# Kernel tuning notes

Hardware: AMD Instinct MI355X
Metric: run time of the kernel (lower is better)

Reference implementation:

```python
import jax, jax.numpy as jnp
import numpy as np

H, DH = 8, 64  # num_heads, head_dim


def setup_inputs() -> dict:
    key = jax.random.key(0)
    ks = jax.random.split(key, 7)
    m, nq, nkv, d = 4, 2048, 2048, 512
    return {
        "xq": jax.random.normal(ks[0], (m, nq, d), jnp.float32),
        "xk": jax.random.normal(ks[1], (m, nkv, d), jnp.float32),
        "xv": jax.random.normal(ks[2], (m, nkv, d), jnp.float32),
        "Wq": jax.random.normal(ks[3], (d, H * DH), jnp.float32) * 0.02,
        "Wk": jax.random.normal(ks[4], (d, H * DH), jnp.float32) * 0.02,
        "Wv": jax.random.normal(ks[5], (d, H * DH), jnp.float32) * 0.02,
        "Wo": jax.random.normal(ks[6], (H * DH, d), jnp.float32) * 0.02,
        "bo": jnp.zeros((d,), jnp.float32),
    }


def _split_heads(t):
    # [b, n, h*d] -> [b, h, n, d]
    b, n, _ = t.shape
    return t.reshape(b, n, H, DH).transpose(0, 2, 1, 3)


def reference(xq, xk, xv, Wq, Wk, Wv, Wo, bo):
    scale = DH ** -0.5
    q = _split_heads(xq @ Wq)   # [b,h,nq,dh]
    k = _split_heads(xk @ Wk)   # [b,h,nkv,dh]
    v = _split_heads(xv @ Wv)   # [b,h,nkv,dh]
    dots = jnp.einsum("bhqd,bhkd->bhqk", q, k) * scale  # [b,h,nq,nkv]
    # diagonal attention term: query attends to its own (k,v) projection
    xq_k = _split_heads(xq @ Wk)
    xq_v = _split_heads(xq @ Wv)
    diag = jnp.sum(q * xq_k, axis=-1, keepdims=True) * scale  # [b,h,nq,1]
    dots = jnp.concatenate([dots, diag], axis=-1)  # [b,h,nq,nkv+1]
    attn = jax.nn.softmax(dots, axis=-1)
    out = jnp.einsum("bhqk,bhkd->bhqd", attn[..., :-1], v) + attn[..., -1:] * xq_v
    b, _, nq, _ = out.shape
    out = out.transpose(0, 2, 1, 3).reshape(b, nq, H * DH)  # merge heads
    return out @ Wo + bo
```

## Files before the change

### kernel.cpp

```cpp
#include <hip/hip_runtime.h>

#define LOG2E 1.44269504088896f
#define CS (0.125f * LOG2E)

typedef __bf16 bf16x8 __attribute__((ext_vector_type(8)));
typedef float f32x4 __attribute__((ext_vector_type(4)));
typedef unsigned short u16x8 __attribute__((ext_vector_type(8)));

__device__ __forceinline__ unsigned short f2bf(float f) {
  union { float f; unsigned int u; } v{f};
  unsigned int r = v.u + 0x7fffu + ((v.u >> 16) & 1u);
  return (unsigned short)(r >> 16);
}
__device__ __forceinline__ float bf2f(unsigned short u) {
  union { unsigned int u; float f; } v; v.u = ((unsigned int)u) << 16; return v.f;
}
__device__ __forceinline__ unsigned int pkr(float a, float b) {
  unsigned int ua = __builtin_bit_cast(unsigned int, a) + 0x8000u;
  unsigned int ub = __builtin_bit_cast(unsigned int, b) + 0x8000u;
  return __builtin_amdgcn_perm(ub, ua, 0x07060302);
}

typedef __attribute__((address_space(3))) unsigned int lds32_t;
typedef const __attribute__((address_space(1))) unsigned int glb32_t;
__device__ __forceinline__ void gld16(const unsigned short* g, unsigned short* l) {
  __builtin_amdgcn_global_load_lds((glb32_t*)(unsigned long long)g,
                                   (lds32_t*)(unsigned int)(unsigned long long)l,
                                   16, 0, 0);
}

__global__ __launch_bounds__(256) void conv_all(
    const float* __restrict__ xq, const float* __restrict__ xk, const float* __restrict__ xv,
    const float* __restrict__ Wq, const float* __restrict__ Wk,
    const float* __restrict__ Wv, const float* __restrict__ Wo,
    unsigned short* __restrict__ oxq, unsigned short* __restrict__ oxk, unsigned short* __restrict__ oxv,
    unsigned short* __restrict__ oWq, unsigned short* __restrict__ oWk,
    unsigned short* __restrict__ oWv, unsigned short* __restrict__ oWo) {
  __shared__ unsigned short T[64 * 65];
  const int blk = blockIdx.x;
  if (blk < 12288) {
    const int N4 = (8192 * 512) / 4;
    int idx = blk * 256 + threadIdx.x;
    const float* src; unsigned short* dst; int i;
    if (idx < N4)          { src = xq; dst = oxq; i = idx; }
    else if (idx < 2 * N4) { src = xk; dst = oxk; i = idx - N4; }
    else                   { src = xv; dst = oxv; i = idx - 2 * N4; }
    float4 v = ((const float4*)src)[i];
    ushort4 o; o.x = f2bf(v.x); o.y = f2bf(v.y); o.z = f2bf(v.z); o.w = f2bf(v.w);
    ((ushort4*)dst)[i] = o;
  } else {
    const int wblk = blk - 12288;
    const int wsel = wblk >> 6;
    const int tile = wblk & 63;
    const int tk = (tile >> 3) * 64, tn = (tile & 7) * 64;
    const float* src = (wsel == 0) ? Wq : (wsel == 1) ? Wk : (wsel == 2) ? Wv : Wo;
    unsigned short* dst = (wsel == 0) ? oWq : (wsel == 1) ? oWk : (wsel == 2) ? oWv : oWo;
    const float scale = (wsel == 0) ? CS : 1.0f;
    const int rr = threadIdx.x >> 4;
    const int cc = (threadIdx.x & 15) * 4;
#pragma unroll
    for (int i = 0; i < 4; i++) {
      int row = rr + i * 16;
      float4 v = *(const float4*)&src[(size_t)(tk + row) * 512 + tn + cc];
      T[(cc + 0) * 65 + row] = f2bf(v.x * scale);
      T[(cc + 1) * 65 + row] = f2bf(v.y * scale);
      T[(cc + 2) * 65 + row] = f2bf(v.z * scale);
      T[(cc + 3) * 65 + row] = f2bf(v.w * scale);
    }
    __syncthreads();
#pragma unroll
    for (int i = 0; i < 4; i++) {
      int n = rr + i * 16;
      ushort4 o;
      o.x = T[n * 65 + cc + 0]; o.y = T[n * 65 + cc + 1];
      o.z = T[n * 65 + cc + 2]; o.w = T[n * 65 + cc + 3];
      *(ushort4*)&dst[(size_t)(tn + n) * 512 + tk + cc] = o;
    }
  }
}

__device__ __forceinline__ void gemm_tile(
    const unsigned short* __restrict__ A, const unsigned short* __restrict__ Bt,
    int rowBlk, int colBlk, unsigned short* As, unsigned short* Bs, f32x4 (&acc)[4][4]) {
  const int t = threadIdx.x;
  const int lane = t & 63, c = lane & 15, g = lane >> 4;
  const int w = t >> 6;
  const int wm = w & 1, wn = w >> 1;
#pragma unroll
  for (int i = 0; i < 4; i++)
#pragma unroll
    for (int j = 0; j < 4; j++)
#pragma unroll
      for (int r = 0; r < 4; r++) acc[i][j][r] = 0.f;

  for (int kk = 0; kk < 512; kk += 32) {
    __syncthreads();
#pragma unroll
    for (int i = 0; i < 2; i++) {
      int idx = t + 256 * i;
      int r = idx >> 2, ch = idx & 3;
      gld16(&A[(size_t)(rowBlk + r) * 512 + kk + ch * 8], &As[idx * 8]);
      gld16(&Bt[(size_t)(colBlk + r) * 512 + kk + ch * 8], &Bs[idx * 8]);
    }
    __syncthreads();
    bf16x8 af[4], bfr[4];
#pragma unroll
    for (int i = 0; i < 4; i++)
      af[i] = __builtin_bit_cast(bf16x8, *(const u16x8*)&As[(wm * 64 + i * 16 + c) * 32 + g * 8]);
#pragma unroll
    for (int j = 0; j < 4; j++)
      bfr[j] = __builtin_bit_cast(bf16x8, *(const u16x8*)&Bs[(wn * 64 + j * 16 + c) * 32 + g * 8]);
#pragma unroll
    for (int i = 0; i < 4; i++)
#pragma unroll
      for (int j = 0; j < 4; j++)
        acc[i][j] = __builtin_amdgcn_mfma_f32_16x16x32_bf16(af[i], bfr[j], acc[i][j], 0, 0, 0);
  }
}

__global__ __launch_bounds__(256) void proj_all(
    const unsigned short* __restrict__ xq, const unsigned short* __restrict__ xk,
    const unsigned short* __restrict__ xv,
    const unsigned short* __restrict__ Wq, const unsigned short* __restrict__ Wk,
    const unsigned short* __restrict__ Wv,
    unsigned short* __restrict__ Qo, unsigned short* __restrict__ XKo,
    unsigned short* __restrict__ XVo, unsigned short* __restrict__ Ko,
    unsigned short* __restrict__ Vto) {
  __shared__ unsigned short As[128 * 32];
  __shared__ unsigned short Bs[128 * 32];
  const int rowBlk = blockIdx.x * 128;
  const int y = blockIdx.y;
  const unsigned short* A; const unsigned short* Bt; int colBlk; int mode;
  unsigned short* out;
  if (y < 12) {
    int wsel = y >> 2;
    A = xq; colBlk = (y & 3) * 128; mode = 0;
    Bt = (wsel == 0) ? Wq : (wsel == 1) ? Wk : Wv;
    out = (wsel == 0) ? Qo : (wsel == 1) ? XKo : XVo;
  } else if (y < 16) {
    A = xk; Bt = Wk; out = Ko; colBlk = (y - 12) * 128; mode = 0;
  } else {
    A = xv; Bt = Wv; out = Vto; colBlk = (y - 16) * 128; mode = 1;
  }
  f32x4 acc[4][4];
  gemm_tile(A, Bt, rowBlk, colBlk, As, Bs, acc);
  const int t = threadIdx.x;
  const int w = t >> 6, lane = t & 63, c = lane & 15, g = lane >> 4;
  const int wm = w & 1, wn = w >> 1;
  if (mode == 0) {
#pragma unroll
    for (int i = 0; i < 4; i++)
#pragma unroll
      for (int j = 0; j < 4; j++)
#pragma unroll
        for (int r = 0; r < 4; r++) {
          int row = rowBlk + wm * 64 + i * 16 + g * 4 + r;
          int col = colBlk + wn * 64 + j * 16 + c;
          out[(size_t)row * 512 + col] = f2bf(acc[i][j][r]);
        }
  } else {
#pragma unroll
    for (int i = 0; i < 4; i++) {
      int tok0 = rowBlk + wm * 64 + i * 16 + g * 4;
      int bb = tok0 >> 11, n0 = tok0 & 2047;
#pragma unroll
      for (int j = 0; j < 4; j++) {
        int col = colBlk + wn * 64 + j * 16 + c;
        int hh = col >> 6, dh = col & 63;
        ushort4 o;
        o.x = f2bf(acc[i][j][0]); o.y = f2bf(acc[i][j][1]);
        o.z = f2bf(acc[i][j][2]); o.w = f2bf(acc[i][j][3]);
        *(ushort4*)&out[((size_t)(bb * 8 + hh) * 64 + dh) * 2048 + n0] = o;
      }
    }
  }
}

__global__ __launch_bounds__(256) void gemm_out(
    const unsigned short* __restrict__ A, const unsigned short* __restrict__ Bt,
    float* __restrict__ out, const float* __restrict__ bias) {
  __shared__ unsigned short As[128 * 32];
  __shared__ unsigned short Bs[64 * 32];
  const int rowBlk = blockIdx.x * 128;
  const int colBlk = blockIdx.y * 64;
  const int t = threadIdx.x;
  const int lane = t & 63, c = lane & 15, g = lane >> 4;
  const int w = t >> 6;
  const int wm = w & 1, wn = w >> 1;
  f32x4 acc[4][2];
#pragma unroll
  for (int i = 0; i < 4; i++)
#pragma unroll
    for (int j = 0; j < 2; j++)
#pragma unroll
      for (int r = 0; r < 4; r++) acc[i][j][r] = 0.f;

  for (int kk = 0; kk < 512; kk += 32) {
    __syncthreads();
#pragma unroll
    for (int i = 0; i < 2; i++) {
      int idx = t + 256 * i;
      int r = idx >> 2, ch = idx & 3;
      gld16(&A[(size_t)(rowBlk + r) * 512 + kk + ch * 8], &As[idx * 8]);
    }
    {
      int r = t >> 2, ch = t & 3;
      gld16(&Bt[(size_t)(colBlk + r) * 512 + kk + ch * 8], &Bs[t * 8]);
    }
    __syncthreads();
    bf16x8 af[4], bfr[2];
#pragma unroll
    for (int i = 0; i < 4; i++)
      af[i] = __builtin_bit_cast(bf16x8, *(const u16x8*)&As[(wm * 64 + i * 16 + c) * 32 + g * 8]);
#pragma unroll
    for (int j = 0; j < 2; j++)
      bfr[j] = __builtin_bit_cast(bf16x8, *(const u16x8*)&Bs[(wn * 32 + j * 16 + c) * 32 + g * 8]);
#pragma unroll
    for (int i = 0; i < 4; i++)
#pragma unroll
      for (int j = 0; j < 2; j++)
        acc[i][j] = __builtin_amdgcn_mfma_f32_16x16x32_bf16(af[i], bfr[j], acc[i][j], 0, 0, 0);
  }
#pragma unroll
  for (int i = 0; i < 4; i++)
#pragma unroll
    for (int j = 0; j < 2; j++)
#pragma unroll
      for (int r = 0; r < 4; r++) {
        int row = rowBlk + wm * 64 + i * 16 + g * 4 + r;
        int col = colBlk + wn * 32 + j * 16 + c;
        out[(size_t)row * 512 + col] = acc[i][j][r] + bias[col];
      }
}

__global__ __launch_bounds__(512, 4) void attn_kernel(
    const unsigned short* __restrict__ Q, const unsigned short* __restrict__ K,
    const unsigned short* __restrict__ Vt, const unsigned short* __restrict__ XK,
    const unsigned short* __restrict__ XV, unsigned short* __restrict__ O) {
  __shared__ unsigned short Ks[64 * 72];
  __shared__ unsigned short Vs[64 * 72];
  __shared__ unsigned short Ps[8][16 * 72];
  __shared__ float Scr[8][32];
  const int t = threadIdx.x;
  const int w = t >> 6, lane = t & 63, c = lane & 15, g = lane >> 4;
  const int qt = blockIdx.x, h = blockIdx.y, b = blockIdx.z;
  const size_t hb = (size_t)b * (2048 * 512) + h * 64;
  const size_t vhb = (size_t)(b * 8 + h) * 64 * 2048;
  const int qbase = qt * 128 + w * 16;
  unsigned short* Pw = &Ps[w][0];

  const int sr = t >> 3, sch = t & 7;
  const size_t kgoff = hb + (size_t)sr * 512 + sch * 8;
  const size_t vgoff = vhb + (size_t)sr * 2048 + sch * 8;
  const int soff = sr * 72 + sch * 8;

  bf16x8 qf[2];
#pragma unroll
  for (int hf = 0; hf < 2; hf++)
    qf[hf] = __builtin_bit_cast(bf16x8,
        *(const u16x8*)&Q[hb + (size_t)(qbase + c) * 512 + hf * 32 + g * 8]);

  f32x4 accO[4];
  float lq = 0.f;
#pragma unroll
  for (int jd = 0; jd < 4; jd++)
#pragma unroll
    for (int r = 0; r < 4; r++) accO[jd][r] = 0.f;

  u16x8 kreg = *(const u16x8*)&K[kgoff];
  u16x8 vreg = *(const u16x8*)&Vt[vgoff];
  *(u16x8*)&Ks[soff] = kreg;
  *(u16x8*)&Vs[soff] = vreg;
  __syncthreads();

  for (int kt = 0; kt < 32; kt++) {
    if (kt < 31) {
      kreg = *(const u16x8*)&K[kgoff + (size_t)(kt + 1) * 64 * 512];
      vreg = *(const u16x8*)&Vt[vgoff + (size_t)(kt + 1) * 64];
    }

    f32x4 s[4];
#pragma unroll
    for (int j = 0; j < 4; j++) {
      bf16x8 kf0 = __builtin_bit_cast(bf16x8, *(const u16x8*)&Ks[(j * 16 + c) * 72 + g * 8]);
      bf16x8 kf1 = __builtin_bit_cast(bf16x8, *(const u16x8*)&Ks[(j * 16 + c) * 72 + 32 + g * 8]);
      f32x4 z; z[0] = z[1] = z[2] = z[3] = 0.f;
      z = __builtin_amdgcn_mfma_f32_16x16x32_bf16(kf0, qf[0], z, 0, 0, 0);
      z = __builtin_amdgcn_mfma_f32_16x16x32_bf16(kf1, qf[1], z, 0, 0, 0);
      s[j] = z;
    }

    float sum = 0.f;
#pragma unroll
    for (int j = 0; j < 4; j++) {
      float p0 = exp2f(s[j][0]);
      float p1 = exp2f(s[j][1]);
      float p2 = exp2f(s[j][2]);
      float p3 = exp2f(s[j][3]);
      sum += (p0 + p1) + (p2 + p3);
      uint2 pw; pw.x = pkr(p0, p1); pw.y = pkr(p2, p3);
      *(uint2*)&Pw[c * 72 + j * 16 + g * 4] = pw;
    }
    lq += sum;

    bf16x8 pf0 = __builtin_bit_cast(bf16x8, *(const u16x8*)&Pw[c * 72 + g * 8]);
    bf16x8 pf1 = __builtin_bit_cast(bf16x8, *(const u16x8*)&Pw[c * 72 + 32 + g * 8]);
#pragma unroll
    for (int jd = 0; jd < 4; jd++) {
      bf16x8 v0 = __builtin_bit_cast(bf16x8, *(const u16x8*)&Vs[(jd * 16 + c) * 72 + g * 8]);
      bf16x8 v1 = __builtin_bit_cast(bf16x8, *(const u16x8*)&Vs[(jd * 16 + c) * 72 + 32 + g * 8]);
      accO[jd] = __builtin_amdgcn_mfma_f32_16x16x32_bf16(pf0, v0, accO[jd], 0, 0, 0);
      accO[jd] = __builtin_amdgcn_mfma_f32_16x16x32_bf16(pf1, v1, accO[jd], 0, 0, 0);
    }

    if (kt < 31) {
      __syncthreads();
      *(u16x8*)&Ks[soff] = kreg;
      *(u16x8*)&Vs[soff] = vreg;
      __syncthreads();
    }
  }

  lq += __shfl_xor(lq, 16);
  lq += __shfl_xor(lq, 32);

  {
    const int qc = qbase + c;
    float part = 0.f;
    {
      const unsigned short* qp = &Q[hb + (size_t)qc * 512 + g * 16];
      const unsigned short* xp = &XK[hb + (size_t)qc * 512 + g * 16];
      u16x8 q0 = *(const u16x8*)&qp[0], q1 = *(const u16x8*)&qp[8];
      u16x8 x0 = *(const u16x8*)&xp[0], x1 = *(const u16x8*)&xp[8];
#pragma unroll
      for (int ii = 0; ii < 8; ii++)
        part += bf2f(q0[ii]) * bf2f(x0[ii]) + bf2f(q1[ii]) * bf2f(x1[ii]);
    }
    part += __shfl_xor(part, 16);
    part += __shfl_xor(part, 32);
    float pd = exp2f(part);
    float inv = 1.f / (lq + pd);
    if (g == 0) {
      Scr[w][c] = inv;
      Scr[w][16 + c] = pd * inv;
    }
    __builtin_amdgcn_s_waitcnt(0);
    f32x4 a4 = *(const f32x4*)&Scr[w][g * 4];
    f32x4 p4 = *(const f32x4*)&Scr[w][16 + g * 4];
#pragma unroll
    for (int jd = 0; jd < 4; jd++)
#pragma unroll
      for (int r = 0; r < 4; r++) {
        int qr = qbase + g * 4 + r;
        float xv = bf2f(XV[hb + (size_t)qr * 512 + jd * 16 + c]);
        float val = accO[jd][r] * a4[r] + p4[r] * xv;
        O[((size_t)(b * 2048 + qr)) * 512 + h * 64 + jd * 16 + c] = f2bf(val);
      }
  }
}

extern "C" void kernel_launch(void* const* d_in, const int* in_sizes, int n_in,
                              void* d_out, int out_size, void* d_ws, size_t ws_size,
                              hipStream_t stream) {
  const float* xq = (const float*)d_in[0];
  const float* xk = (const float*)d_in[1];
  const float* xv = (const float*)d_in[2];
  const float* Wq = (const float*)d_in[3];
  const float* Wk = (const float*)d_in[4];
  const float* Wv = (const float*)d_in[5];
  const float* Wo = (const float*)d_in[6];
  const float* bo = (const float*)d_in[7];

  unsigned short* ws = (unsigned short*)d_ws;
  const size_t MD = 8192ull * 512;
  const size_t WD = 512ull * 512;
  unsigned short* xq_b = ws;
  unsigned short* xk_b = xq_b + MD;
  unsigned short* xv_b = xk_b + MD;
  unsigned short* Wq_t = xv_b + MD;
  unsigned short* Wk_t = Wq_t + WD;
  unsigned short* Wv_t = Wk_t + WD;
  unsigned short* Wo_t = Wv_t + WD;
  unsigned short* Qb  = Wo_t + WD;
  unsigned short* Kb  = Qb + MD;
  unsigned short* Vtb = Kb + MD;
  unsigned short* XKb = Vtb + MD;
  unsigned short* XVb = XKb + MD;
  unsigned short* Ob  = XVb + MD;

  conv_all<<<dim3(12544), 256, 0, stream>>>(xq, xk, xv, Wq, Wk, Wv, Wo,
                                            xq_b, xk_b, xv_b, Wq_t, Wk_t, Wv_t, Wo_t);
  proj_all<<<dim3(64, 20), 256, 0, stream>>>(xq_b, xk_b, xv_b, Wq_t, Wk_t, Wv_t,
                                             Qb, XKb, XVb, Kb, Vtb);
  attn_kernel<<<dim3(16, 8, 4), 512, 0, stream>>>(Qb, Kb, Vtb, XKb, XVb, Ob);
  gemm_out<<<dim3(64, 8), 256, 0, stream>>>(Ob, Wo_t, (float*)d_out, bo);
}
```

Before: 216.1 us.

## Double-buffer K/V tiles with direct global-to-LDS loads and XOR swizzle

```diff
diff --git a/kernel.cpp b/kernel.cpp
--- a/kernel.cpp
+++ b/kernel.cpp
@@ -6,6 +6,13 @@
 typedef __bf16 bf16x8 __attribute__((ext_vector_type(8)));
 typedef float f32x4 __attribute__((ext_vector_type(4)));
 typedef unsigned short u16x8 __attribute__((ext_vector_type(8)));
+
+#if __has_builtin(__builtin_amdgcn_exp2f)
+#define fexp2(x) __builtin_amdgcn_exp2f(x)
+#else
+extern "C" __device__ float __ocml_native_exp2_f32(float);
+#define fexp2(x) __ocml_native_exp2_f32(x)
+#endif
 
 __device__ __forceinline__ unsigned short f2bf(float f) {
   union { float f; unsigned int u; } v{f};
@@ -237,8 +244,8 @@
     const unsigned short* __restrict__ Q, const unsigned short* __restrict__ K,
     const unsigned short* __restrict__ Vt, const unsigned short* __restrict__ XK,
     const unsigned short* __restrict__ XV, unsigned short* __restrict__ O) {
-  __shared__ unsigned short Ks[64 * 72];
-  __shared__ unsigned short Vs[64 * 72];
+  __shared__ unsigned short Ks[2][64 * 64];
+  __shared__ unsigned short Vs[2][64 * 64];
   __shared__ unsigned short Ps[8][16 * 72];
   __shared__ float Scr[8][32];
   const int t = threadIdx.x;
@@ -250,9 +257,12 @@
   unsigned short* Pw = &Ps[w][0];
 
   const int sr = t >> 3, sch = t & 7;
-  const size_t kgoff = hb + (size_t)sr * 512 + sch * 8;
-  const size_t vgoff = vhb + (size_t)sr * 2048 + sch * 8;
-  const int soff = sr * 72 + sch * 8;
+  const int ssl = (sch ^ (sr & 7)) * 8;
+  const size_t kgoff = hb + (size_t)sr * 512 + ssl;
+  const size_t vgoff = vhb + (size_t)sr * 2048 + ssl;
+
+  const int sw0 = ((g ^ (c & 7)) << 3);
+  const int sw1 = (((g | 4) ^ (c & 7)) << 3);
 
   bf16x8 qf[2];
 #pragma unroll
@@ -267,36 +277,39 @@
 #pragma unroll
     for (int r = 0; r < 4; r++) accO[jd][r] = 0.f;
 
-  u16x8 kreg = *(const u16x8*)&K[kgoff];
-  u16x8 vreg = *(const u16x8*)&Vt[vgoff];
-  *(u16x8*)&Ks[soff] = kreg;
-  *(u16x8*)&Vs[soff] = vreg;
+  gld16(&K[kgoff], &Ks[0][t * 8]);
+  gld16(&Vt[vgoff], &Vs[0][t * 8]);
   __syncthreads();
 
+  int cur = 0;
   for (int kt = 0; kt < 32; kt++) {
     if (kt < 31) {
-      kreg = *(const u16x8*)&K[kgoff + (size_t)(kt + 1) * 64 * 512];
-      vreg = *(const u16x8*)&Vt[vgoff + (size_t)(kt + 1) * 64];
-    }
+      gld16(&K[kgoff + (size_t)(kt + 1) * (64 * 512)], &Ks[cur ^ 1][t * 8]);
+      gld16(&Vt[vgoff + (size_t)(kt + 1) * 64], &Vs[cur ^ 1][t * 8]);
+    }
+    const unsigned short* Kc = &Ks[cur][0];
+    const unsigned short* Vc = &Vs[cur][0];
 
     f32x4 s[4];
+    __builtin_amdgcn_s_setprio(1);
 #pragma unroll
     for (int j = 0; j < 4; j++) {
-      bf16x8 kf0 = __builtin_bit_cast(bf16x8, *(const u16x8*)&Ks[(j * 16 + c) * 72 + g * 8]);
-      bf16x8 kf1 = __builtin_bit_cast(bf16x8, *(const u16x8*)&Ks[(j * 16 + c) * 72 + 32 + g * 8]);
+      bf16x8 kf0 = __builtin_bit_cast(bf16x8, *(const u16x8*)&Kc[(j * 16 + c) * 64 + sw0]);
+      bf16x8 kf1 = __builtin_bit_cast(bf16x8, *(const u16x8*)&Kc[(j * 16 + c) * 64 + sw1]);
       f32x4 z; z[0] = z[1] = z[2] = z[3] = 0.f;
       z = __builtin_amdgcn_mfma_f32_16x16x32_bf16(kf0, qf[0], z, 0, 0, 0);
       z = __builtin_amdgcn_mfma_f32_16x16x32_bf16(kf1, qf[1], z, 0, 0, 0);
       s[j] = z;
     }
+    __builtin_amdgcn_s_setprio(0);
 
     float sum = 0.f;
 #pragma unroll
     for (int j = 0; j < 4; j++) {
-      float p0 = exp2f(s[j][0]);
-      float p1 = exp2f(s[j][1]);
-      float p2 = exp2f(s[j][2]);
-      float p3 = exp2f(s[j][3]);
+      float p0 = fexp2(s[j][0]);
+      float p1 = fexp2(s[j][1]);
+      float p2 = fexp2(s[j][2]);
+      float p3 = fexp2(s[j][3]);
       sum += (p0 + p1) + (p2 + p3);
       uint2 pw; pw.x = pkr(p0, p1); pw.y = pkr(p2, p3);
       *(uint2*)&Pw[c * 72 + j * 16 + g * 4] = pw;
@@ -305,20 +318,18 @@
 
     bf16x8 pf0 = __builtin_bit_cast(bf16x8, *(const u16x8*)&Pw[c * 72 + g * 8]);
     bf16x8 pf1 = __builtin_bit_cast(bf16x8, *(const u16x8*)&Pw[c * 72 + 32 + g * 8]);
+    __builtin_amdgcn_s_setprio(1);
 #pragma unroll
     for (int jd = 0; jd < 4; jd++) {
-      bf16x8 v0 = __builtin_bit_cast(bf16x8, *(const u16x8*)&Vs[(jd * 16 + c) * 72 + g * 8]);
-      bf16x8 v1 = __builtin_bit_cast(bf16x8, *(const u16x8*)&Vs[(jd * 16 + c) * 72 + 32 + g * 8]);
+      bf16x8 v0 = __builtin_bit_cast(bf16x8, *(const u16x8*)&Vc[(jd * 16 + c) * 64 + sw0]);
+      bf16x8 v1 = __builtin_bit_cast(bf16x8, *(const u16x8*)&Vc[(jd * 16 + c) * 64 + sw1]);
       accO[jd] = __builtin_amdgcn_mfma_f32_16x16x32_bf16(pf0, v0, accO[jd], 0, 0, 0);
       accO[jd] = __builtin_amdgcn_mfma_f32_16x16x32_bf16(pf1, v1, accO[jd], 0, 0, 0);
     }
-
-    if (kt < 31) {
-      __syncthreads();
-      *(u16x8*)&Ks[soff] = kreg;
-      *(u16x8*)&Vs[soff] = vreg;
-      __syncthreads();
-    }
+    __builtin_amdgcn_s_setprio(0);
+
+    if (kt < 31) __syncthreads();
+    cur ^= 1;
   }
 
   lq += __shfl_xor(lq, 16);
@@ -338,7 +349,7 @@
     }
     part += __shfl_xor(part, 16);
     part += __shfl_xor(part, 32);
-    float pd = exp2f(part);
+    float pd = fexp2(part);
     float inv = 1.f / (lq + pd);
     if (g == 0) {
       Scr[w][c] = inv;
```

After: 205.9 us. 4.7% less time.
